# Performance work log

Measured on AMD Instinct MI355X. Metric: run time of the kernel, lower is better.

Reference implementation:

```python
import jax, jax.numpy as jnp
import numpy as np

NUM_ENT = 50000
NUM_REL = 500
K = 50            # chosenrelnum == number of anchors
D1, D2 = 20, 20   # emb_dim1, emb_dim2
EMB = D1 * D2     # 400
FEAT = 1000
N_NODES = NUM_ENT + NUM_REL
N_EDGES = 400000
B = 4096
CONV = D1 * D2 * 8 // 2  # 1600 = conv_size


def _xavier(key, shape):
    s = (6.0 / (shape[0] + shape[1])) ** 0.5
    return jax.random.uniform(key, shape, jnp.float32, -s, s)


def setup_inputs():
    key = jax.random.key(0)
    ks = jax.random.split(key, 16)
    return {
        "num_feature": jax.random.normal(ks[0], (N_NODES, FEAT), jnp.float32),
        "anchor_num_feature": jax.random.normal(ks[1], (K, FEAT), jnp.float32),
        "Wp": _xavier(ks[2], (1, FEAT)),            # rel2prob
        "bp": jnp.zeros((1,), jnp.float32),
        "Wa": _xavier(ks[3], (FEAT, FEAT)),         # convAnchor2Rel1
        "ba": jnp.zeros((FEAT,), jnp.float32),
        "W1": _xavier(ks[4], (FEAT, EMB)),          # conv1
        "b1": jnp.zeros((EMB,), jnp.float32),
        "ent_emb": _xavier(ks[5], (NUM_ENT, EMB)),
        "rel_emb": _xavier(ks[6], (NUM_REL, EMB)),
        "conv_w": _xavier(ks[7], (8, 3)),           # Conv3d(1,8,(1,1,3)) kernel
        "conv_b": jnp.zeros((8,), jnp.float32),
        "fc_w": _xavier(ks[8], (1, CONV)),          # fc_layer
        "fc_b": jnp.zeros((1,), jnp.float32),
        "edge_index": jax.random.randint(ks[9], (2, N_EDGES), 0, N_NODES),
        "relanchor_edge_index": jax.random.randint(ks[10], (2, 2000), 0, 2 * K),
        "r_idx": jax.random.randint(ks[11], (B,), 0, NUM_REL),
        "e1_idx": jax.random.randint(ks[12], (B,), 0, NUM_ENT),
        "e2_idx": jax.random.randint(ks[13], (B,), 0, NUM_ENT),
    }


def _gcn(x, ei, W, b):
    # torch_geometric GCNConv: sym-normalized aggregation with self loops, bias after aggr
    n = x.shape[0]
    xw = x @ W
    src, dst = ei[0], ei[1]
    deg = jnp.zeros((n,), x.dtype).at[dst].add(1.0) + 1.0  # +1 for self loop
    dinv = jax.lax.rsqrt(deg)
    msg = xw[src] * (dinv[src] * dinv[dst])[:, None]       # [E, out]
    out = jnp.zeros_like(xw).at[dst].add(msg) + xw * (dinv * dinv)[:, None]
    return out + b


def _forward(num_feature, anchor_num_feature, Wp, bp, Wa, ba, W1, b1,
             ent_emb, rel_emb, conv_w, conv_b, fc_w, fc_b,
             edge_index, relanchor_edge_index, r_idx, e1_idx, e2_idx):
    # --- HGNN: relation-prob routing (topk) + anchor GCN + scatter update ---
    rel_feat = num_feature[:NUM_REL - 1]                       # [R-1, FEAT]
    prob = jax.nn.softmax(rel_feat @ Wp.T + bp, axis=0)        # softmax over relations
    rel_feat = rel_feat * prob
    _, idx = jax.lax.top_k(prob[:, 0], K)
    idx = jnp.sort(idx)
    rel1 = rel_feat[idx]                                       # [K, FEAT]
    ra = jnp.concatenate([anchor_num_feature, rel1], axis=0)   # [2K, FEAT]
    x1 = jax.nn.relu(_gcn(ra, relanchor_edge_index, Wa, ba))   # dropout = identity (eval)
    temp = num_feature.at[idx].set(x1[K:])                     # scatter-update of embeddings
    x = jax.nn.relu(_gcn(num_feature, edge_index, W1, b1))     # [N, EMB]
    # --- conv3d multi-branch scorer, arity-2 (len(batch)==3) branch ---
    r = rel_emb[r_idx].reshape(-1, D1, D2)
    e1 = ent_emb[e1_idx].reshape(-1, D1, D2)
    e2 = ent_emb[e2_idx].reshape(-1, D1, D2)
    cube = jnp.stack([r, e1, e2], axis=-1)                     # [B, D1, D2, 3]; bn1 eval = identity
    h = jnp.einsum('bhwk,ok->bohw', cube, conv_w) + conv_b[None, :, None, None]
    h = h.reshape(-1, 4, 2, D1, D2).max(axis=2)                # MaxPool3d((2,1,1)) over 8 channels
    score = h.reshape(-1, CONV) @ fc_w.T + fc_b                # [B, 1]
    return score, x, temp


def reference(num_feature, anchor_num_feature, Wp, bp, Wa, ba, W1, b1,
              ent_emb, rel_emb, conv_w, conv_b, fc_w, fc_b,
              edge_index, relanchor_edge_index, r_idx, e1_idx, e2_idx):
    return _forward(num_feature, anchor_num_feature, Wp, bp, Wa, ba, W1, b1,
                    ent_emb, rel_emb, conv_w, conv_b, fc_w, fc_b,
                    edge_index, relanchor_edge_index, r_idx, e1_idx, e2_idx)
```

## Files before the change

### kernel.cpp

```cpp
#include <hip/hip_runtime.h>
#include <hip/hip_bf16.h>

#define NUM_ENT   50000
#define NUM_RELC  500
#define KTOP      50
#define EMB       400
#define FEAT      1000
#define N_NODES   50500
#define N_EDGES   400000
#define BATCH     4096
#define RELM1     499

#define KP   1024
#define MP   50560
#define NP   512

#define NB_SCAN ((N_NODES + 255) / 256)
#define NB_HIST ((N_EDGES + 255) / 256)

typedef __attribute__((ext_vector_type(8))) short short8;
typedef __attribute__((ext_vector_type(4))) float f32x4;

__device__ __forceinline__ ushort f2bf(float x) {
    __hip_bfloat16 h = __float2bfloat16(x);
    return *reinterpret_cast<ushort*>(&h);
}
__device__ __forceinline__ float bflo(uint u) { return __uint_as_float(u << 16); }
__device__ __forceinline__ float bfhi(uint u) { return __uint_as_float(u & 0xffff0000u); }

#define NCC      4096
#define PB_LOG   RELM1
#define PB_TWA   (PB_LOG + 256)
#define PB_TW1   (PB_TWA + 128)
#define PB_HIST  (PB_TW1 + NB_HIST)
#define PB_TOTAL (PB_HIST + 1)
__global__ void mega1_kernel(const float* __restrict__ nf, float* __restrict__ temp,
                             ushort* __restrict__ Abf,
                             const float* __restrict__ Wp, const float* __restrict__ bp,
                             float* __restrict__ logits,
                             const float* __restrict__ Wa, ushort* __restrict__ Watbf,
                             const float* __restrict__ W1, ushort* __restrict__ Btbf,
                             const int* __restrict__ edge_index, int* __restrict__ cnt,
                             const int* __restrict__ ra_edge, float* __restrict__ dinv_s,
                             int* __restrict__ offs_sm, int* __restrict__ es_sm) {
    __shared__ float tile[64][65];
    int blk = blockIdx.x, t = threadIdx.x;
    if (blk < NCC) {
        size_t idx = (size_t)blk * 256 + t;
        size_t stride = (size_t)NCC * 256;
        size_t total = (size_t)MP * KP / 8;
        for (; idx < total; idx += stride) {
            int row = (int)(idx >> 7);
            int kb  = (int)(idx & 127);
            if (row < N_NODES && kb < 125) {
                size_t off = (size_t)row * FEAT + kb * 8;
                float4 a = *(const float4*)&nf[off];
                float4 b = *(const float4*)&nf[off + 4];
                *(float4*)&temp[off]     = a;
                *(float4*)&temp[off + 4] = b;
                ushort v[8];
                v[0] = f2bf(a.x); v[1] = f2bf(a.y); v[2] = f2bf(a.z); v[3] = f2bf(a.w);
                v[4] = f2bf(b.x); v[5] = f2bf(b.y); v[6] = f2bf(b.z); v[7] = f2bf(b.w);
                *(uint4*)&Abf[idx * 8] = *(uint4*)v;
            } else {
                uint4 z = {0u, 0u, 0u, 0u};
                *(uint4*)&Abf[idx * 8] = z;
            }
        }
        return;
    }
    int b = blk - NCC;
    if (b < PB_LOG) {
        float* red = &tile[0][0];
        float s = 0.f;
        for (int k = t; k < FEAT; k += 256) s += nf[(size_t)b * FEAT + k] * Wp[k];
        red[t] = s; __syncthreads();
        for (int st = 128; st > 0; st >>= 1) { if (t < st) red[t] += red[t + st]; __syncthreads(); }
        if (t == 0) logits[b] = red[0] + bp[0];
    } else if (b < PB_TW1) {
        const float* src; ushort* dst; int K, N, bb;
        if (b < PB_TWA) { bb = b - PB_LOG; src = Wa; dst = Watbf; K = FEAT; N = FEAT; }
        else            { bb = b - PB_TWA; src = W1; dst = Btbf;  K = FEAT; N = EMB;  }
        int k0 = (bb & 15) * 64, n0 = (bb >> 4) * 64;
        int tx = t & 63, ty = t >> 6;
        for (int i = ty; i < 64; i += 4) {
            int k = k0 + i, n = n0 + tx;
            tile[i][tx] = (k < K && n < N) ? src[(size_t)k * N + n] : 0.f;
        }
        __syncthreads();
        for (int i = ty; i < 64; i += 4) {
            int n = n0 + i, k = k0 + tx;
            dst[(size_t)n * KP + k] = f2bf(tile[tx][i]);
        }
    } else if (b < PB_HIST) {
        int e = (b - PB_TW1) * 256 + t;
        if (e < N_EDGES) atomicAdd(&cnt[edge_index[N_EDGES + e]], 1);
    } else {
        __shared__ int c[128];
        __shared__ int o50[64];
        __shared__ int cur[64];
        if (t < 128) c[t] = 0;
        if (t < 64)  cur[t] = 0;
        __syncthreads();
        for (int e = t; e < 2000; e += 256) atomicAdd(&c[ra_edge[2000 + e]], 1);
        __syncthreads();
        if (t < 2 * KTOP) dinv_s[t] = rsqrtf((float)c[t] + 1.0f);
        if (t == 0) {
            int run = 0;
            for (int j = 0; j < KTOP; j++) { o50[j] = run; run += c[KTOP + j]; }
            o50[KTOP] = run;
        }
        __syncthreads();
        if (t < KTOP + 1) offs_sm[t] = o50[t];
        for (int e = t; e < 2000; e += 256) {
            int dst = ra_edge[2000 + e];
            if (dst >= KTOP) {
                int pos = o50[dst - KTOP] + atomicAdd(&cur[dst - KTOP], 1);
                es_sm[pos] = ra_edge[e];
            }
        }
    }
}

__global__ void mega2_kernel(const float* __restrict__ logits,
                             const float* __restrict__ anchor, const float* __restrict__ nf,
                             ushort* __restrict__ rabf,
                             int* __restrict__ idxbuf, float* __restrict__ probsel,
                             const int* __restrict__ cnt, int* __restrict__ offs,
                             int* __restrict__ partials, float* __restrict__ dinv) {
    int blk = blockIdx.x, t = threadIdx.x;
    if (blk < 128) {
        __shared__ float l[RELM1];
        __shared__ float p[RELM1];
        __shared__ int   fl[RELM1];
        __shared__ float red[256];
        __shared__ int   pick;
        __shared__ float pickp;
        int r = blk;
        float v1 = (t < RELM1) ? logits[t] : -1e30f;
        float v2 = (t + 256 < RELM1) ? logits[t + 256] : -1e30f;
        if (t < RELM1) l[t] = v1;
        if (t + 256 < RELM1) l[t + 256] = v2;
        red[t] = fmaxf(v1, v2); __syncthreads();
        for (int s = 128; s > 0; s >>= 1) { if (t < s) red[t] = fmaxf(red[t], red[t + s]); __syncthreads(); }
        float m = red[0]; __syncthreads();
        float e1 = (t < RELM1) ? expf(v1 - m) : 0.f;
        float e2 = (t + 256 < RELM1) ? expf(v2 - m) : 0.f;
        red[t] = e1 + e2; __syncthreads();
        for (int s = 128; s > 0; s >>= 1) { if (t < s) red[t] += red[t + s]; __syncthreads(); }
        float denom = red[0];
        if (t < RELM1) p[t] = e1 / denom;
        if (t + 256 < RELM1) p[t + 256] = e2 / denom;
        __syncthreads();
        #pragma unroll
        for (int h = 0; h < 2; h++) {
            int i = t + h * 256;
            if (i < RELM1) {
                float li = l[i]; int c = 0;
                for (int j = 0; j < RELM1; j++) {
                    float lj = l[j];
                    c += (lj > li) || (lj == li && j < i);
                }
                fl[i] = (c < KTOP) ? 1 : 0;
            }
        }
        __syncthreads();
        if (t == 0) pick = -1;
        __syncthreads();
        int want = r - KTOP;
        #pragma unroll
        for (int h = 0; h < 2; h++) {
            int i = t + h * 256;
            if (i < RELM1 && fl[i]) {
                int rank = 0;
                for (int j = 0; j < i; j++) rank += fl[j];
                if (r == 0) { idxbuf[rank] = i; probsel[rank] = p[i]; }
                if (rank == want) { pick = i; pickp = p[i]; }
            }
        }
        __syncthreads();
        const float* src = nullptr; float scale = 1.f;
        if (r < KTOP) { src = anchor + (size_t)r * FEAT; }
        else if (r < 2 * KTOP) { src = nf + (size_t)pick * FEAT; scale = pickp; }
        for (int k = t; k < KP; k += 256) {
            float v = (src != nullptr && k < FEAT) ? src[k] * scale : 0.f;
            rabf[(size_t)r * KP + k] = f2bf(v);
        }
    } else {
        __shared__ int s[256];
        int b = blk - 128;
        int i = b * 256 + t;
        int v = (i < N_NODES) ? cnt[i] : 0;
        if (i < N_NODES) dinv[i] = rsqrtf((float)v + 1.0f);
        s[t] = v; __syncthreads();
        for (int off = 1; off < 256; off <<= 1) {
            int add = (t >= off) ? s[t - off] : 0;
            __syncthreads();
            s[t] += add;
            __syncthreads();
        }
        if (i < N_NODES) offs[i] = s[t] - v;
        if (t == 255) partials[b] = s[t];
    }
}

__global__ void scan_carry_add(int* __restrict__ offs, const int* __restrict__ partials) {
    __shared__ int s[256];
    int b = blockIdx.x, t = threadIdx.x;
    int v = (t < NB_SCAN) ? partials[t] : 0;
    s[t] = v; __syncthreads();
    for (int off = 1; off < 256; off <<= 1) {
        int add = (t >= off) ? s[t - off] : 0;
        __syncthreads();
        s[t] += add;
        __syncthreads();
    }
    int carry = (b == 0) ? 0 : s[b - 1];
    int i = b * 256 + t;
    if (i < N_NODES && carry) offs[i] += carry;
}

template <typename OutT, bool PACK5>
__device__ __forceinline__ void gemm_body(const ushort* __restrict__ A,
                                          const ushort* __restrict__ Bt,
                                          OutT* __restrict__ C,
                                          int M, int N, int ldc,
                                          int orig, int nwg,
                                          ushort* As, ushort* Bs, int t) {
    int q = nwg >> 3, r8 = nwg & 7;
    int xcd = orig & 7;
    int wgid = (xcd < r8 ? xcd * (q + 1) : r8 * (q + 1) + (xcd - r8) * q) + (orig >> 3);
    int ntiles = PACK5 ? 3 : ((N + 127) >> 7);
    int n0 = (wgid % ntiles) * 128;
    int m0 = (wgid / ntiles) * 128;

    int srow = t >> 3;
    int kbx  = (t & 7) ^ (srow & 7);
    int lane = t & 63;
    int wv   = t >> 6;
    int wr   = wv >> 1, wc = wv & 1;
    int l15  = lane & 15, lhi = lane >> 4;

    f32x4 acc[4][5];
    #pragma unroll
    for (int m = 0; m < 4; m++)
        #pragma unroll
        for (int n = 0; n < 5; n++) acc[m][n] = (f32x4){0.f, 0.f, 0.f, 0.f};

    for (int kt = 0; kt < KP / 64; kt++) {
        int k0 = kt * 64;
        #pragma unroll
        for (int r = 0; r < 4; r++) {
            int row = r * 32 + srow;
            const ushort* ga = A  + (size_t)(m0 + row) * KP + k0 + kbx * 8;
            const ushort* gb = Bt + (size_t)(n0 + row) * KP + k0 + kbx * 8;
            ushort* la = &As[(size_t)row * 64 + (t & 7) * 8];
            ushort* lb = &Bs[(size_t)row * 64 + (t & 7) * 8];
            __builtin_amdgcn_global_load_lds(
                (const __attribute__((address_space(1))) unsigned int*)ga,
                (__attribute__((address_space(3))) unsigned int*)la, 16, 0, 0);
            __builtin_amdgcn_global_load_lds(
                (const __attribute__((address_space(1))) unsigned int*)gb,
                (__attribute__((address_space(3))) unsigned int*)lb, 16, 0, 0);
        }
        if (PACK5) {
            if (n0 == 256 && t < 128) {
                int row = 128 + srow;
                const ushort* gb = Bt + (size_t)(n0 + row) * KP + k0 + kbx * 8;
                ushort* lb = &Bs[(size_t)row * 64 + (t & 7) * 8];
                __builtin_amdgcn_global_load_lds(
                    (const __attribute__((address_space(1))) unsigned int*)gb,
                    (__attribute__((address_space(3))) unsigned int*)lb, 16, 0, 0);
            }
        }
        __syncthreads();

        #pragma unroll
        for (int ks = 0; ks < 2; ks++) {
            int cswz = ((ks * 64 + lhi * 16) ^ ((lane & 7) << 4)) >> 1;
            short8 af[4], bfr[5];
            #pragma unroll
            for (int m = 0; m < 4; m++) {
                int rowl = wr * 64 + m * 16 + l15;
                af[m] = *(const short8*)&As[rowl * 64 + cswz];
            }
            #pragma unroll
            for (int n = 0; n < 5; n++) {
                bool valid = PACK5 ? ((n < 4) || (wc == 1 && n0 == 256))
                                   : ((n < 4) && (n0 + wc * 64 + n * 16 < N));
                if (valid) {
                    int rowl = wc * 64 + n * 16 + l15;
                    bfr[n] = *(const short8*)&Bs[rowl * 64 + cswz];
                }
            }
            #pragma unroll
            for (int m = 0; m < 4; m++)
                #pragma unroll
                for (int n = 0; n < 5; n++) {
                    bool valid = PACK5 ? ((n < 4) || (wc == 1 && n0 == 256))
                                       : ((n < 4) && (n0 + wc * 64 + n * 16 < N));
                    if (valid)
                        acc[m][n] = __builtin_amdgcn_mfma_f32_16x16x32_bf16(
                            af[m], bfr[n], acc[m][n], 0, 0, 0);
                }
        }
        __syncthreads();
    }

    #pragma unroll
    for (int m = 0; m < 4; m++) {
        #pragma unroll
        for (int n = 0; n < 5; n++) {
            bool valid = PACK5 ? ((n < 4) || (wc == 1 && n0 == 256))
                               : ((n < 4) && (n0 + wc * 64 + n * 16 < N));
            if (!valid) continue;
            int gc = n0 + wc * 64 + n * 16 + l15;
            if (gc >= N) continue;
            int gr0 = m0 + wr * 64 + m * 16 + lhi * 4;
            #pragma unroll
            for (int j = 0; j < 4; j++) {
                int gr = gr0 + j;
                if (gr < M) {
                    if constexpr (sizeof(OutT) == 2)
                        C[(size_t)gr * ldc + gc] = (OutT)f2bf(acc[m][n][j]);
                    else
                        C[(size_t)gr * ldc + gc] = (OutT)acc[m][n][j];
                }
            }
        }
    }
}

#define NBIG ((MP / 128) * 3)
#define M3_GS (NBIG + 8)
#define M3_TOTAL (M3_GS + NB_HIST)
__global__ __launch_bounds__(256) void mega3_kernel(
        const ushort* __restrict__ Abf, const ushort* __restrict__ Btbf,
        ushort* __restrict__ xwb,
        const ushort* __restrict__ rabf, const ushort* __restrict__ Watbf,
        float* __restrict__ raw,
        const int* __restrict__ ei, const int* __restrict__ offs,
        int* __restrict__ cursor, const float* __restrict__ dinv,
        int* __restrict__ esrc, float* __restrict__ ecoef) {
    __shared__ ushort As[128 * 64];
    __shared__ ushort Bs[144 * 64];
    int blk = blockIdx.x, t = threadIdx.x;
    if (blk < NBIG) {
        gemm_body<ushort, true>(Abf, Btbf, xwb, N_NODES, EMB, EMB, blk, NBIG, As, Bs, t);
    } else if (blk < M3_GS) {
        gemm_body<float, false>(rabf, Watbf, raw, 2 * KTOP, FEAT, FEAT, blk - NBIG, 8,
                                As, Bs, t);
    } else {
        int e = (blk - M3_GS) * 256 + t;
        if (e >= N_EDGES) return;
        int src = ei[e], dst = ei[N_EDGES + e];
        int pos = offs[dst] + atomicAdd(&cursor[dst], 1);
        esrc[pos] = src;
        ecoef[pos] = dinv[src] * dinv[dst];
    }
}

#define EB_GB ((N_NODES + 3) / 4)
#define EB_GS (EB_GB + KTOP)
#define EB_TOTAL (EB_GS + BATCH / 4)
__global__ __launch_bounds__(256) void epilogue_kernel(
        const int* __restrict__ esrc, const float* __restrict__ ecoef,
        const int* __restrict__ offs, const int* __restrict__ cnt,
        const ushort* __restrict__ xwb, const float* __restrict__ dinv,
        const float* __restrict__ b1, float* __restrict__ x,
        const int* __restrict__ es_sm, const int* __restrict__ offs_sm,
        const float* __restrict__ raw, const float* __restrict__ dinv_s,
        const float* __restrict__ ba, const int* __restrict__ idxbuf,
        float* __restrict__ temp,
        const float* __restrict__ ent, const float* __restrict__ rel,
        const int* __restrict__ r_idx, const int* __restrict__ e1_idx,
        const int* __restrict__ e2_idx, const float* __restrict__ conv_w,
        const float* __restrict__ conv_b, const float* __restrict__ fc_w,
        const float* __restrict__ fc_b, float* __restrict__ out) {
    int blk = blockIdx.x, t = threadIdx.x;
    if (blk < EB_GB) {
        int wave = t >> 6, lane = t & 63;
        int dst = blk * 4 + wave;
        if (dst >= N_NODES) return;
        int start = offs[dst], deg = cnt[dst];
        bool act = lane < EMB / 8;
        float acc[8] = {};
        int j = 0;
        for (; j + 1 < deg; j += 2) {
            int s0 = esrc[start + j], s1 = esrc[start + j + 1];
            float c0 = ecoef[start + j], c1 = ecoef[start + j + 1];
            if (act) {
                uint4 u0 = *(const uint4*)(xwb + (size_t)s0 * EMB + lane * 8);
                uint4 u1 = *(const uint4*)(xwb + (size_t)s1 * EMB + lane * 8);
                acc[0] += bflo(u0.x) * c0 + bflo(u1.x) * c1;
                acc[1] += bfhi(u0.x) * c0 + bfhi(u1.x) * c1;
                acc[2] += bflo(u0.y) * c0 + bflo(u1.y) * c1;
                acc[3] += bfhi(u0.y) * c0 + bfhi(u1.y) * c1;
                acc[4] += bflo(u0.z) * c0 + bflo(u1.z) * c1;
                acc[5] += bfhi(u0.z) * c0 + bfhi(u1.z) * c1;
                acc[6] += bflo(u0.w) * c0 + bflo(u1.w) * c1;
                acc[7] += bfhi(u0.w) * c0 + bfhi(u1.w) * c1;
            }
        }
        if (j < deg) {
            int s0 = esrc[start + j];
            float c0 = ecoef[start + j];
            if (act) {
                uint4 u0 = *(const uint4*)(xwb + (size_t)s0 * EMB + lane * 8);
                acc[0] += bflo(u0.x) * c0; acc[1] += bfhi(u0.x) * c0;
                acc[2] += bflo(u0.y) * c0; acc[3] += bfhi(u0.y) * c0;
                acc[4] += bflo(u0.z) * c0; acc[5] += bfhi(u0.z) * c0;
                acc[6] += bflo(u0.w) * c0; acc[7] += bfhi(u0.w) * c0;
            }
        }
        if (!act) return;
        float d2 = dinv[dst] * dinv[dst];
        uint4 u = *(const uint4*)(xwb + (size_t)dst * EMB + lane * 8);
        const float* bp = b1 + lane * 8;
        float* xo = x + (size_t)dst * EMB + lane * 8;
        float4 o0, o1;
        o0.x = fmaxf(acc[0] + bflo(u.x) * d2 + bp[0], 0.f);
        o0.y = fmaxf(acc[1] + bfhi(u.x) * d2 + bp[1], 0.f);
        o0.z = fmaxf(acc[2] + bflo(u.y) * d2 + bp[2], 0.f);
        o0.w = fmaxf(acc[3] + bfhi(u.y) * d2 + bp[3], 0.f);
        o1.x = fmaxf(acc[4] + bflo(u.z) * d2 + bp[4], 0.f);
        o1.y = fmaxf(acc[5] + bfhi(u.z) * d2 + bp[5], 0.f);
        o1.z = fmaxf(acc[6] + bflo(u.w) * d2 + bp[6], 0.f);
        o1.w = fmaxf(acc[7] + bfhi(u.w) * d2 + bp[7], 0.f);
        *(float4*)&xo[0] = o0;
        *(float4*)&xo[4] = o1;
    } else if (blk < EB_GS) {
        int j = blk - EB_GB;
        int r = KTOP + j;
        int start = offs_sm[j], end = offs_sm[j + 1];
        float dr = dinv_s[r];
        float acc[4] = {};
        for (int p = start; p < end; p++) {
            int src = es_sm[p];
            float cc = dinv_s[src] * dr;
            const float* rs = raw + (size_t)src * FEAT;
            #pragma unroll
            for (int qq = 0; qq < 4; qq++) {
                int k = t + qq * 256;
                if (k < FEAT) acc[qq] += rs[k] * cc;
            }
        }
        float d2 = dr * dr;
        const float* rd = raw + (size_t)r * FEAT;
        float* to = temp + (size_t)idxbuf[j] * FEAT;
        #pragma unroll
        for (int qq = 0; qq < 4; qq++) {
            int k = t + qq * 256;
            if (k < FEAT) to[k] = fmaxf(acc[qq] + rd[k] * d2 + ba[k], 0.f);
        }
    } else {
        __shared__ float cw[24];
        __shared__ float cb[8];
        if (t < 24) cw[t] = conv_w[t];
        if (t < 8)  cb[t] = conv_b[t];
        __syncthreads();
        int wave = t >> 6, lane = t & 63;
        int b = (blk - EB_GS) * 4 + wave;
        if (b >= BATCH) return;
        const float* r  = rel + (size_t)r_idx[b] * EMB;
        const float* e1 = ent + (size_t)e1_idx[b] * EMB;
        const float* e2 = ent + (size_t)e2_idx[b] * EMB;
        float partial = 0.f;
        for (int p = lane; p < EMB; p += 64) {
            float c0 = r[p], c1 = e1[p], c2 = e2[p];
            for (int g = 0; g < 4; g++) {
                float h0 = c0 * cw[(2 * g) * 3 + 0] + c1 * cw[(2 * g) * 3 + 1] + c2 * cw[(2 * g) * 3 + 2] + cb[2 * g];
                float h1 = c0 * cw[(2 * g + 1) * 3 + 0] + c1 * cw[(2 * g + 1) * 3 + 1] + c2 * cw[(2 * g + 1) * 3 + 2] + cb[2 * g + 1];
                partial += fmaxf(h0, h1) * fc_w[g * EMB + p];
            }
        }
        for (int off = 32; off > 0; off >>= 1) partial += __shfl_down(partial, off, 64);
        if (lane == 0) out[b] = partial + fc_b[0];
    }
}

extern "C" void kernel_launch(void* const* d_in, const int* in_sizes, int n_in,
                              void* d_out, int out_size, void* d_ws, size_t ws_size,
                              hipStream_t stream) {
    const float* num_feature = (const float*)d_in[0];
    const float* anchor      = (const float*)d_in[1];
    const float* Wp          = (const float*)d_in[2];
    const float* bp          = (const float*)d_in[3];
    const float* Wa          = (const float*)d_in[4];
    const float* ba          = (const float*)d_in[5];
    const float* W1          = (const float*)d_in[6];
    const float* b1          = (const float*)d_in[7];
    const float* ent_emb     = (const float*)d_in[8];
    const float* rel_emb     = (const float*)d_in[9];
    const float* conv_w      = (const float*)d_in[10];
    const float* conv_b      = (const float*)d_in[11];
    const float* fc_w        = (const float*)d_in[12];
    const float* fc_b        = (const float*)d_in[13];
    const int*   edge_index  = (const int*)d_in[14];
    const int*   ra_edge     = (const int*)d_in[15];
    const int*   r_idx       = (const int*)d_in[16];
    const int*   e1_idx      = (const int*)d_in[17];
    const int*   e2_idx      = (const int*)d_in[18];

    float* out_score = (float*)d_out;
    float* out_x     = out_score + BATCH;
    float* out_temp  = out_x + (size_t)N_NODES * EMB;

    float* ws_f     = (float*)d_ws;
    float* logits   = ws_f;
    int*   idxbuf   = (int*)(ws_f + 512);
    float* probsel  = ws_f + 576;
    float* dinv_s   = ws_f + 640;
    int*   offs_sm  = (int*)(ws_f + 768);
    int*   es_sm    = (int*)(ws_f + 832);
    float* raw      = ws_f + 2880;
    float* dinv     = ws_f + 102880;
    ushort* rabf    = (ushort*)(ws_f + 153380);
    ushort* Btbf    = (ushort*)(ws_f + 218916);
    ushort* Watbf   = (ushort*)(ws_f + 481060);
    int*   cnt      = (int*)(ws_f + 1005348);
    int*   cursor   = cnt + N_NODES;
    int*   offs     = cursor + N_NODES;
    int*   partials = offs + N_NODES;
    int*   esrc     = partials + 256;
    float* ecoef    = (float*)(esrc + N_EDGES);
    ushort* Abf     = (ushort*)(ecoef + N_EDGES);
    ushort* xwb     = Abf + (size_t)MP * KP;

    hipMemsetAsync(cnt, 0, 2 * N_NODES * sizeof(int), stream);

    mega1_kernel<<<NCC + PB_TOTAL, 256, 0, stream>>>(
        num_feature, out_temp, Abf, Wp, bp, logits, Wa, Watbf, W1, Btbf,
        edge_index, cnt, ra_edge, dinv_s, offs_sm, es_sm);

    mega2_kernel<<<128 + NB_SCAN, 256, 0, stream>>>(
        logits, anchor, num_feature, rabf, idxbuf, probsel,
        cnt, offs, partials, dinv);

    scan_carry_add<<<NB_SCAN, 256, 0, stream>>>(offs, partials);

    mega3_kernel<<<M3_TOTAL, 256, 0, stream>>>(
        Abf, Btbf, xwb, rabf, Watbf, raw,
        edge_index, offs, cursor, dinv, esrc, ecoef);

    epilogue_kernel<<<EB_TOTAL, 256, 0, stream>>>(
        esrc, ecoef, offs, cnt, xwb, dinv, b1, out_x,
        es_sm, offs_sm, raw, dinv_s, ba, idxbuf, out_temp,
        ent_emb, rel_emb, r_idx, e1_idx, e2_idx, conv_w, conv_b, fc_w, fc_b,
        out_score);
}
```

Measured before the change: 374.9 us.

## Merge scan, rabf, carry and GEMM kernels into one ticket-ordered megakernel

Replaces mega2, scan_carry_add and mega3 with a single launch. Blocks take an atomic ticket so dependent roles are ordered, and they wait on agent-scope atomic counters (scan done, rabf done, carry done, offsets done) instead of kernel boundaries. The goal is to remove two launch gaps and the tail idle time between them, so the big GEMM can overlap with the scan and softmax work. In exchange, waiting blocks spin and hold CU slots, and the scheme relies on the ticket ordering to avoid deadlock.

```diff
diff --git a/kernel.cpp b/kernel.cpp
--- a/kernel.cpp
+++ b/kernel.cpp
@@ -17,6 +17,7 @@
 
 #define NB_SCAN ((N_NODES + 255) / 256)
 #define NB_HIST ((N_EDGES + 255) / 256)
+#define NBIG    ((MP / 128) * 3)
 
 typedef __attribute__((ext_vector_type(8))) short short8;
 typedef __attribute__((ext_vector_type(4))) float f32x4;
@@ -27,6 +28,19 @@
 }
 __device__ __forceinline__ float bflo(uint u) { return __uint_as_float(u << 16); }
 __device__ __forceinline__ float bfhi(uint u) { return __uint_as_float(u & 0xffff0000u); }
+
+__device__ __forceinline__ void wait_ge(int* p, int target) {
+    while (__hip_atomic_load(p, __ATOMIC_ACQUIRE, __HIP_MEMORY_SCOPE_AGENT) < target)
+        __builtin_amdgcn_s_sleep(2);
+}
+__device__ __forceinline__ void signal_add(int* p) {
+    __hip_atomic_fetch_add(p, 1, __ATOMIC_RELEASE, __HIP_MEMORY_SCOPE_AGENT);
+}
+#define SY_TICKET 0
+#define SY_SCAN   1
+#define SY_RABF   2
+#define SY_CARRY  3
+#define SY_OFFS   4
 
 #define NCC      4096
 #define PB_LOG   RELM1
@@ -122,104 +136,6 @@
     }
 }
 
-__global__ void mega2_kernel(const float* __restrict__ logits,
-                             const float* __restrict__ anchor, const float* __restrict__ nf,
-                             ushort* __restrict__ rabf,
-                             int* __restrict__ idxbuf, float* __restrict__ probsel,
-                             const int* __restrict__ cnt, int* __restrict__ offs,
-                             int* __restrict__ partials, float* __restrict__ dinv) {
-    int blk = blockIdx.x, t = threadIdx.x;
-    if (blk < 128) {
-        __shared__ float l[RELM1];
-        __shared__ float p[RELM1];
-        __shared__ int   fl[RELM1];
-        __shared__ float red[256];
-        __shared__ int   pick;
-        __shared__ float pickp;
-        int r = blk;
-        float v1 = (t < RELM1) ? logits[t] : -1e30f;
-        float v2 = (t + 256 < RELM1) ? logits[t + 256] : -1e30f;
-        if (t < RELM1) l[t] = v1;
-        if (t + 256 < RELM1) l[t + 256] = v2;
-        red[t] = fmaxf(v1, v2); __syncthreads();
-        for (int s = 128; s > 0; s >>= 1) { if (t < s) red[t] = fmaxf(red[t], red[t + s]); __syncthreads(); }
-        float m = red[0]; __syncthreads();
-        float e1 = (t < RELM1) ? expf(v1 - m) : 0.f;
-        float e2 = (t + 256 < RELM1) ? expf(v2 - m) : 0.f;
-        red[t] = e1 + e2; __syncthreads();
-        for (int s = 128; s > 0; s >>= 1) { if (t < s) red[t] += red[t + s]; __syncthreads(); }
-        float denom = red[0];
-        if (t < RELM1) p[t] = e1 / denom;
-        if (t + 256 < RELM1) p[t + 256] = e2 / denom;
-        __syncthreads();
-        #pragma unroll
-        for (int h = 0; h < 2; h++) {
-            int i = t + h * 256;
-            if (i < RELM1) {
-                float li = l[i]; int c = 0;
-                for (int j = 0; j < RELM1; j++) {
-                    float lj = l[j];
-                    c += (lj > li) || (lj == li && j < i);
-                }
-                fl[i] = (c < KTOP) ? 1 : 0;
-            }
-        }
-        __syncthreads();
-        if (t == 0) pick = -1;
-        __syncthreads();
-        int want = r - KTOP;
-        #pragma unroll
-        for (int h = 0; h < 2; h++) {
-            int i = t + h * 256;
-            if (i < RELM1 && fl[i]) {
-                int rank = 0;
-                for (int j = 0; j < i; j++) rank += fl[j];
-                if (r == 0) { idxbuf[rank] = i; probsel[rank] = p[i]; }
-                if (rank == want) { pick = i; pickp = p[i]; }
-            }
-        }
-        __syncthreads();
-        const float* src = nullptr; float scale = 1.f;
-        if (r < KTOP) { src = anchor + (size_t)r * FEAT; }
-        else if (r < 2 * KTOP) { src = nf + (size_t)pick * FEAT; scale = pickp; }
-        for (int k = t; k < KP; k += 256) {
-            float v = (src != nullptr && k < FEAT) ? src[k] * scale : 0.f;
-            rabf[(size_t)r * KP + k] = f2bf(v);
-        }
-    } else {
-        __shared__ int s[256];
-        int b = blk - 128;
-        int i = b * 256 + t;
-        int v = (i < N_NODES) ? cnt[i] : 0;
-        if (i < N_NODES) dinv[i] = rsqrtf((float)v + 1.0f);
-        s[t] = v; __syncthreads();
-        for (int off = 1; off < 256; off <<= 1) {
-            int add = (t >= off) ? s[t - off] : 0;
-            __syncthreads();
-            s[t] += add;
-            __syncthreads();
-        }
-        if (i < N_NODES) offs[i] = s[t] - v;
-        if (t == 255) partials[b] = s[t];
-    }
-}
-
-__global__ void scan_carry_add(int* __restrict__ offs, const int* __restrict__ partials) {
-    __shared__ int s[256];
-    int b = blockIdx.x, t = threadIdx.x;
-    int v = (t < NB_SCAN) ? partials[t] : 0;
-    s[t] = v; __syncthreads();
-    for (int off = 1; off < 256; off <<= 1) {
-        int add = (t >= off) ? s[t - off] : 0;
-        __syncthreads();
-        s[t] += add;
-        __syncthreads();
-    }
-    int carry = (b == 0) ? 0 : s[b - 1];
-    int i = b * 256 + t;
-    if (i < N_NODES && carry) offs[i] += carry;
-}
-
 template <typename OutT, bool PACK5>
 __device__ __forceinline__ void gemm_body(const ushort* __restrict__ A,
                                           const ushort* __restrict__ Bt,
@@ -331,27 +247,141 @@
     }
 }
 
-#define NBIG ((MP / 128) * 3)
-#define M3_GS (NBIG + 8)
-#define M3_TOTAL (M3_GS + NB_HIST)
-__global__ __launch_bounds__(256) void mega3_kernel(
+#define TK_RABF0 198
+#define TK_CARRY 326
+#define TK_OFFS0 327
+#define TK_GBIG0 525
+#define TK_GSM0  (TK_GBIG0 + NBIG)
+#define TK_CSR0  (TK_GSM0 + 8)
+#define TK_TOTAL (TK_CSR0 + NB_HIST)
+__global__ __launch_bounds__(256) void megaX_kernel(
+        int* __restrict__ sync,
+        const float* __restrict__ logits,
+        const float* __restrict__ anchor, const float* __restrict__ nf,
+        ushort* __restrict__ rabf, int* __restrict__ idxbuf, float* __restrict__ probsel,
+        const int* __restrict__ cnt, int* __restrict__ offs,
+        int* __restrict__ partials, float* __restrict__ dinv,
         const ushort* __restrict__ Abf, const ushort* __restrict__ Btbf,
         ushort* __restrict__ xwb,
-        const ushort* __restrict__ rabf, const ushort* __restrict__ Watbf,
-        float* __restrict__ raw,
-        const int* __restrict__ ei, const int* __restrict__ offs,
-        int* __restrict__ cursor, const float* __restrict__ dinv,
+        const ushort* __restrict__ Watbf, float* __restrict__ raw,
+        const int* __restrict__ ei, int* __restrict__ cursor,
         int* __restrict__ esrc, float* __restrict__ ecoef) {
     __shared__ ushort As[128 * 64];
     __shared__ ushort Bs[144 * 64];
-    int blk = blockIdx.x, t = threadIdx.x;
-    if (blk < NBIG) {
-        gemm_body<ushort, true>(Abf, Btbf, xwb, N_NODES, EMB, EMB, blk, NBIG, As, Bs, t);
-    } else if (blk < M3_GS) {
-        gemm_body<float, false>(rabf, Watbf, raw, 2 * KTOP, FEAT, FEAT, blk - NBIG, 8,
-                                As, Bs, t);
+    __shared__ int tk_s;
+    int t = threadIdx.x;
+    if (t == 0) tk_s = atomicAdd(&sync[SY_TICKET], 1);
+    __syncthreads();
+    int tk = tk_s;
+
+    if (tk < TK_RABF0) {
+        int* s = (int*)As;
+        int b = tk;
+        int i = b * 256 + t;
+        int v = (i < N_NODES) ? cnt[i] : 0;
+        if (i < N_NODES) dinv[i] = rsqrtf((float)v + 1.0f);
+        s[t] = v; __syncthreads();
+        for (int off = 1; off < 256; off <<= 1) {
+            int add = (t >= off) ? s[t - off] : 0;
+            __syncthreads();
+            s[t] += add;
+            __syncthreads();
+        }
+        if (i < N_NODES) offs[i] = s[t] - v;
+        if (t == 255) partials[b] = s[t];
+        __syncthreads();
+        if (t == 0) { __threadfence(); signal_add(&sync[SY_SCAN]); }
+    } else if (tk < TK_CARRY) {
+        float* l   = (float*)As;
+        float* p   = l + 512;
+        int*   fl  = (int*)(l + 1024);
+        float* red = l + 1536;
+        __shared__ int   pick;
+        __shared__ float pickp;
+        int r = tk - TK_RABF0;
+        float v1 = (t < RELM1) ? logits[t] : -1e30f;
+        float v2 = (t + 256 < RELM1) ? logits[t + 256] : -1e30f;
+        if (t < RELM1) l[t] = v1;
+        if (t + 256 < RELM1) l[t + 256] = v2;
+        red[t] = fmaxf(v1, v2); __syncthreads();
+        for (int s = 128; s > 0; s >>= 1) { if (t < s) red[t] = fmaxf(red[t], red[t + s]); __syncthreads(); }
+        float m = red[0]; __syncthreads();
+        float e1 = (t < RELM1) ? expf(v1 - m) : 0.f;
+        float e2 = (t + 256 < RELM1) ? expf(v2 - m) : 0.f;
+        red[t] = e1 + e2; __syncthreads();
+        for (int s = 128; s > 0; s >>= 1) { if (t < s) red[t] += red[t + s]; __syncthreads(); }
+        float denom = red[0];
+        if (t < RELM1) p[t] = e1 / denom;
+        if (t + 256 < RELM1) p[t + 256] = e2 / denom;
+        __syncthreads();
+        #pragma unroll
+        for (int h = 0; h < 2; h++) {
+            int i = t + h * 256;
+            if (i < RELM1) {
+                float li = l[i]; int c = 0;
+                for (int j = 0; j < RELM1; j++) {
+                    float lj = l[j];
+                    c += (lj > li) || (lj == li && j < i);
+                }
+                fl[i] = (c < KTOP) ? 1 : 0;
+            }
+        }
+        __syncthreads();
+        if (t == 0) pick = -1;
+        __syncthreads();
+        int want = r - KTOP;
+        #pragma unroll
+        for (int h = 0; h < 2; h++) {
+            int i = t + h * 256;
+            if (i < RELM1 && fl[i]) {
+                int rank = 0;
+                for (int j = 0; j < i; j++) rank += fl[j];
+                if (r == 0) { idxbuf[rank] = i; probsel[rank] = p[i]; }
+                if (rank == want) { pick = i; pickp = p[i]; }
+            }
+        }
+        __syncthreads();
+        const float* src = nullptr; float scale = 1.f;
+        if (r < KTOP) { src = anchor + (size_t)r * FEAT; }
+        else if (r < 2 * KTOP) { src = nf + (size_t)pick * FEAT; scale = pickp; }
+        for (int k = t; k < KP; k += 256) {
+            float v = (src != nullptr && k < FEAT) ? src[k] * scale : 0.f;
+            rabf[(size_t)r * KP + k] = f2bf(v);
+        }
+        __syncthreads();
+        if (t == 0) { __threadfence(); signal_add(&sync[SY_RABF]); }
+    } else if (tk == TK_CARRY) {
+        wait_ge(&sync[SY_SCAN], NB_SCAN);
+        int* s = (int*)As;
+        int v = (t < NB_SCAN) ? partials[t] : 0;
+        s[t] = v; __syncthreads();
+        for (int off = 1; off < 256; off <<= 1) {
+            int add = (t >= off) ? s[t - off] : 0;
+            __syncthreads();
+            s[t] += add;
+            __syncthreads();
+        }
+        if (t < NB_SCAN) partials[t] = s[t] - v;
+        __syncthreads();
+        if (t == 0) { __threadfence(); signal_add(&sync[SY_CARRY]); }
+    } else if (tk < TK_GBIG0) {
+        wait_ge(&sync[SY_CARRY], 1);
+        int b = tk - TK_OFFS0;
+        int carry = partials[b];
+        int i = b * 256 + t;
+        if (i < N_NODES && carry) offs[i] += carry;
+        __syncthreads();
+        if (t == 0) { __threadfence(); signal_add(&sync[SY_OFFS]); }
+    } else if (tk < TK_GSM0) {
+        gemm_body<ushort, true>(Abf, Btbf, xwb, N_NODES, EMB, EMB,
+                                tk - TK_GBIG0, NBIG, As, Bs, t);
+    } else if (tk < TK_CSR0) {
+        wait_ge(&sync[SY_RABF], 128);
+        gemm_body<float, false>(rabf, Watbf, raw, 2 * KTOP, FEAT, FEAT,
+                                tk - TK_GSM0, 8, As, Bs, t);
     } else {
-        int e = (blk - M3_GS) * 256 + t;
+        wait_ge(&sync[SY_OFFS], NB_SCAN);
+        int e = (tk - TK_CSR0) * 256 + t;
         if (e >= N_EDGES) return;
         int src = ei[e], dst = ei[N_EDGES + e];
         int pos = offs[dst] + atomicAdd(&cursor[dst], 1);
@@ -513,12 +543,13 @@
     float* dinv_s   = ws_f + 640;
     int*   offs_sm  = (int*)(ws_f + 768);
     int*   es_sm    = (int*)(ws_f + 832);
-    float* raw      = ws_f + 2880;
-    float* dinv     = ws_f + 102880;
-    ushort* rabf    = (ushort*)(ws_f + 153380);
-    ushort* Btbf    = (ushort*)(ws_f + 218916);
-    ushort* Watbf   = (ushort*)(ws_f + 481060);
-    int*   cnt      = (int*)(ws_f + 1005348);
+    int*   sync     = (int*)(ws_f + 2880);
+    float* raw      = ws_f + 2896;
+    float* dinv     = ws_f + 102896;
+    ushort* rabf    = (ushort*)(ws_f + 153396);
+    ushort* Btbf    = (ushort*)(ws_f + 218932);
+    ushort* Watbf   = (ushort*)(ws_f + 481076);
+    int*   cnt      = (int*)(ws_f + 1005364);
     int*   cursor   = cnt + N_NODES;
     int*   offs     = cursor + N_NODES;
     int*   partials = offs + N_NODES;
@@ -528,20 +559,16 @@
     ushort* xwb     = Abf + (size_t)MP * KP;
 
     hipMemsetAsync(cnt, 0, 2 * N_NODES * sizeof(int), stream);
+    hipMemsetAsync(sync, 0, 16 * sizeof(int), stream);
 
     mega1_kernel<<<NCC + PB_TOTAL, 256, 0, stream>>>(
         num_feature, out_temp, Abf, Wp, bp, logits, Wa, Watbf, W1, Btbf,
         edge_index, cnt, ra_edge, dinv_s, offs_sm, es_sm);
 
-    mega2_kernel<<<128 + NB_SCAN, 256, 0, stream>>>(
-        logits, anchor, num_feature, rabf, idxbuf, probsel,
-        cnt, offs, partials, dinv);
-
-    scan_carry_add<<<NB_SCAN, 256, 0, stream>>>(offs, partials);
-
-    mega3_kernel<<<M3_TOTAL, 256, 0, stream>>>(
-        Abf, Btbf, xwb, rabf, Watbf, raw,
-        edge_index, offs, cursor, dinv, esrc, ecoef);
+    megaX_kernel<<<TK_TOTAL, 256, 0, stream>>>(
+        sync, logits, anchor, num_feature, rabf, idxbuf, probsel,
+        cnt, offs, partials, dinv, Abf, Btbf, xwb, Watbf, raw,
+        edge_index, cursor, esrc, ecoef);
 
     epilogue_kernel<<<EB_TOTAL, 256, 0, stream>>>(
         esrc, ecoef, offs, cnt, xwb, dinv, b1, out_x,
```

Result: slower. 506.4 us (+35.1%).
